# Performance work log

Measured on AMD Instinct MI355X. Metric: run time of the kernel, lower is better.

Reference implementation:

```python
import jax, jax.numpy as jnp
import numpy as np

DIM = 1024
N_HEADS = 16
HEAD_DIM = DIM // N_HEADS


def setup_inputs() -> dict:
    key = jax.random.key(0)
    k_x, k_qkv_w, k_qkv_b, k_p_w, k_p_b = jax.random.split(key, 5)
    s = 1.0 / np.sqrt(DIM)
    return {
        "x": jax.random.normal(k_x, (2, 2048, DIM), dtype=jnp.float32),
        # stored as [in, out] so forward is x @ W + b (equivalent to torch Linear)
        "qkv_w": jax.random.uniform(k_qkv_w, (DIM, 3 * DIM), minval=-s, maxval=s, dtype=jnp.float32),
        "qkv_b": jax.random.uniform(k_qkv_b, (3 * DIM,), minval=-s, maxval=s, dtype=jnp.float32),
        "proj_w": jax.random.uniform(k_p_w, (DIM, DIM), minval=-s, maxval=s, dtype=jnp.float32),
        "proj_b": jax.random.uniform(k_p_b, (DIM,), minval=-s, maxval=s, dtype=jnp.float32),
    }


def reference(x, qkv_w, qkv_b, proj_w, proj_b):
    b, s, _ = x.shape
    qkv = x @ qkv_w + qkv_b                       # [b, s, 3*dim]
    q, k, v = jnp.split(qkv, 3, axis=-1)
    def split_heads(t):
        return t.reshape(b, s, N_HEADS, HEAD_DIM).transpose(0, 2, 1, 3)  # [b, h, s, d]
    q, k, v = map(split_heads, (q, k, v))
    scale = 1.0 / np.sqrt(HEAD_DIM)
    scores = jnp.einsum("bhqd,bhkd->bhqk", q, k) * scale
    attn = jax.nn.softmax(scores, axis=-1)
    out = jnp.einsum("bhqk,bhkd->bhqd", attn, v)
    out = out.transpose(0, 2, 1, 3).reshape(b, s, DIM)
    return out @ proj_w + proj_b
```

## Files before the change

### kernel.cpp

```cpp
#include <hip/hip_runtime.h>
#include <hip/hip_bf16.h>

typedef __attribute__((ext_vector_type(8))) short bf16x8;
typedef __attribute__((ext_vector_type(4))) float f32x4;
typedef __attribute__((ext_vector_type(16))) float f32x16;
typedef __attribute__((ext_vector_type(4))) unsigned short u16x4;
typedef __attribute__((ext_vector_type(8))) unsigned short u16x8v;

#define S_LEN 2048
#define NHEAD 16
#define HDIM 64
#define DIM 1024

__device__ __forceinline__ unsigned short f2bf(float f) {
    union { float f; unsigned u; } x; x.f = f;
    unsigned r = x.u + 0x7FFFu + ((x.u >> 16) & 1u);
    return (unsigned short)(r >> 16);
}
__device__ __forceinline__ unsigned short f2bf_fast(float f) {
    union { float f; unsigned u; } x; x.f = f;
    return (unsigned short)((x.u + 0x8000u) >> 16);
}

__device__ __forceinline__ f32x4 mfma16(bf16x8 a, bf16x8 b, f32x4 c) {
    return __builtin_amdgcn_mfma_f32_16x16x32_bf16(a, b, c, 0, 0, 0);
}
__device__ __forceinline__ f32x16 mfma32(bf16x8 a, bf16x8 b, f32x16 c) {
    return __builtin_amdgcn_mfma_f32_32x32x16_bf16(a, b, c, 0, 0, 0);
}

__device__ __forceinline__ float fexp2(float x) {
#if __has_builtin(__builtin_amdgcn_exp2f)
    return __builtin_amdgcn_exp2f(x);
#else
    return exp2f(x);
#endif
}

__device__ __forceinline__ void gl_lds16(const void* g, void* l) {
    __builtin_amdgcn_global_load_lds(
        (const __attribute__((address_space(1))) unsigned int*)g,
        (__attribute__((address_space(3))) unsigned int*)l, 16, 0, 0);
}

__global__ __launch_bounds__(256) void xconv_kernel(const float* __restrict__ X,
                                                    unsigned short* __restrict__ Xb) {
    size_t i = ((size_t)blockIdx.x * 256 + threadIdx.x) * 8;
    float4 a = *reinterpret_cast<const float4*>(&X[i]);
    float4 b = *reinterpret_cast<const float4*>(&X[i + 4]);
    u16x8v o;
    o[0] = f2bf(a.x); o[1] = f2bf(a.y); o[2] = f2bf(a.z); o[3] = f2bf(a.w);
    o[4] = f2bf(b.x); o[5] = f2bf(b.y); o[6] = f2bf(b.z); o[7] = f2bf(b.w);
    *reinterpret_cast<u16x8v*>(&Xb[i]) = o;
}

__global__ __launch_bounds__(256) void wtrans_kernel(const float* __restrict__ W,
                                                     unsigned short* __restrict__ Wt,
                                                     int K, int N) {
    __shared__ float lds[64][65];
    int k0 = blockIdx.x * 64, n0 = blockIdx.y * 64;
    int tid = threadIdx.x;
    for (int idx = tid; idx < 1024; idx += 256) {
        int row = idx >> 4, c = (idx & 15) << 2;
        float4 v = *reinterpret_cast<const float4*>(&W[(size_t)(k0 + row) * N + n0 + c]);
        lds[row][c] = v.x; lds[row][c + 1] = v.y; lds[row][c + 2] = v.z; lds[row][c + 3] = v.w;
    }
    __syncthreads();
    for (int idx = tid; idx < 1024; idx += 256) {
        int row = idx >> 4, c = (idx & 15) << 2;
        u16x4 o;
        o[0] = f2bf(lds[c][row]);     o[1] = f2bf(lds[c + 1][row]);
        o[2] = f2bf(lds[c + 2][row]); o[3] = f2bf(lds[c + 3][row]);
        *reinterpret_cast<u16x4*>(&Wt[(size_t)(n0 + row) * K + k0 + c]) = o;
    }
}

template <int MODE>
__global__ __launch_bounds__(256) void gemm_kernel(
    const unsigned short* __restrict__ Ab, const unsigned short* __restrict__ Bt,
    const float* __restrict__ bias,
    unsigned short* __restrict__ Qb, unsigned short* __restrict__ Kb,
    unsigned short* __restrict__ Vt, float* __restrict__ outf) {
    __shared__ unsigned short Alds[128 * 64];
    __shared__ unsigned short Blds[128 * 64];
    const int tid = threadIdx.x;
    const int m0 = blockIdx.x * 128, n0 = blockIdx.y * 128;
    const int wid = tid >> 6, lane = tid & 63;
    const int wm = wid >> 1, wn = wid & 1;
    const int lr = lane & 15, lg = lane >> 4;

    const char* Abase = (const char*)(Ab + (size_t)m0 * 1024);
    const char* Bbase = (const char*)(Bt + (size_t)n0 * 1024);

    int srcOff[4], dstOff[4];
#pragma unroll
    for (int i = 0; i < 4; ++i) {
        int off = i * 4096 + wid * 1024 + lane * 16;
        int row = off >> 7, col = off & 127;
        srcOff[i] = row * 2048 + (col ^ ((row & 7) << 4));
        dstOff[i] = off;
    }
    const int swz = (lr & 7) << 4;

    f32x4 acc[4][4] = {};

    for (int kt = 0; kt < 16; ++kt) {
        __syncthreads();
#pragma unroll
        for (int i = 0; i < 4; ++i) {
            gl_lds16(Abase + srcOff[i] + kt * 128, (char*)Alds + dstOff[i]);
            gl_lds16(Bbase + srcOff[i] + kt * 128, (char*)Blds + dstOff[i]);
        }
        __syncthreads();

#pragma unroll
        for (int ks = 0; ks < 2; ++ks) {
            bf16x8 af[4], bfr[4];
#pragma unroll
            for (int i = 0; i < 4; ++i)
                af[i] = *reinterpret_cast<const bf16x8*>(
                    (const char*)Alds + (wm * 64 + i * 16 + lr) * 128 + ((ks * 64 + lg * 16) ^ swz));
#pragma unroll
            for (int j = 0; j < 4; ++j)
                bfr[j] = *reinterpret_cast<const bf16x8*>(
                    (const char*)Blds + (wn * 64 + j * 16 + lr) * 128 + ((ks * 64 + lg * 16) ^ swz));
            __builtin_amdgcn_s_setprio(1);
#pragma unroll
            for (int i = 0; i < 4; ++i)
#pragma unroll
                for (int j = 0; j < 4; ++j)
                    acc[i][j] = mfma16(af[i], bfr[j], acc[i][j]);
            __builtin_amdgcn_s_setprio(0);
        }
    }

    if constexpr (MODE == 0) {
        const int sec = n0 >> 10;
#pragma unroll
        for (int j = 0; j < 4; ++j) {
            int gn = n0 + wn * 64 + j * 16 + lr;
            float bv = bias[gn];
            int nn = gn & 1023, h = nn >> 6, d = nn & 63;
#pragma unroll
            for (int i = 0; i < 4; ++i) {
#pragma unroll
                for (int r = 0; r < 4; ++r) {
                    int m = m0 + wm * 64 + i * 16 + lg * 4 + r;
                    int b_ = m >> 11, s_ = m & 2047;
                    size_t bh = (size_t)(b_ * NHEAD + h);
                    float v = acc[i][j][r] + bv;
                    if (sec == 0)
                        Qb[(bh * S_LEN + s_) * HDIM + d] = f2bf(v * 0.18033688f);
                    else if (sec == 1)
                        Kb[(bh * S_LEN + s_) * HDIM + d] = f2bf(v);
                    else
                        Vt[(bh * HDIM + d) * S_LEN + s_] = f2bf(v);
                }
            }
        }
    } else {
#pragma unroll
        for (int j = 0; j < 4; ++j) {
            int gn = n0 + wn * 64 + j * 16 + lr;
            float bv = bias[gn];
#pragma unroll
            for (int i = 0; i < 4; ++i) {
#pragma unroll
                for (int r = 0; r < 4; ++r) {
                    int m = m0 + wm * 64 + i * 16 + lg * 4 + r;
                    outf[(size_t)m * DIM + gn] = acc[i][j][r] + bv;
                }
            }
        }
    }
}

#define NT (S_LEN / 64)
__global__ __launch_bounds__(256) void attn_kernel(const unsigned short* __restrict__ Qb,
                                                   const unsigned short* __restrict__ Kb,
                                                   const unsigned short* __restrict__ Vt,
                                                   unsigned short* __restrict__ Ob) {
    __shared__ unsigned short Klds[2][64 * 64];
    __shared__ unsigned short Vlds[2][64 * 64];
    const int bh = blockIdx.y;
    const int wid = threadIdx.x >> 6;
    const int lane = threadIdx.x & 63;
    const int l31 = lane & 31, hi = lane >> 5;
    const int q0 = blockIdx.x * 128 + wid * 32;

    const unsigned short* qrow = &Qb[((size_t)bh * S_LEN + q0 + l31) * HDIM];
    bf16x8 qf[4];
#pragma unroll
    for (int kst = 0; kst < 4; ++kst)
        qf[kst] = *reinterpret_cast<const bf16x8*>(&qrow[kst * 16 + hi * 8]);

    const char* kT = (const char*)&Kb[(size_t)bh * S_LEN * HDIM];
    const char* vT = (const char*)&Vt[(size_t)bh * HDIM * S_LEN];

    const int Lb0 = (wid * 2 + 0) * 1024 + lane * 16;
    const int Lb1 = (wid * 2 + 1) * 1024 + lane * 16;
    const int row0 = Lb0 >> 7, row1 = Lb1 >> 7;
    const int sw0 = (Lb0 & 127) ^ ((row0 & 7) << 4);
    const int sw1 = (Lb1 & 127) ^ ((row1 & 7) << 4);
    const int dst0 = wid * 2048, dst1 = wid * 2048 + 1024;

    const int swz = (l31 & 7) << 4;

    float ls = 0.f;
    f32x16 acc[2] = {};

    {
        char* kl = (char*)Klds[0]; char* vl = (char*)Vlds[0];
        gl_lds16(kT + row0 * 128 + sw0, kl + dst0);
        gl_lds16(kT + row1 * 128 + sw1, kl + dst1);
        gl_lds16(vT + row0 * 4096 + sw0, vl + dst0);
        gl_lds16(vT + row1 * 4096 + sw1, vl + dst1);
    }

    int cur = 0;
    for (int jt = 0; jt < NT; ++jt) {
        __syncthreads();
        if (jt + 1 < NT) {
            char* kl = (char*)Klds[cur ^ 1]; char* vl = (char*)Vlds[cur ^ 1];
            size_t kof = (size_t)(jt + 1) * 8192, vof = (size_t)(jt + 1) * 128;
            gl_lds16(kT + kof + row0 * 128 + sw0, kl + dst0);
            gl_lds16(kT + kof + row1 * 128 + sw1, kl + dst1);
            gl_lds16(vT + vof + row0 * 4096 + sw0, vl + dst0);
            gl_lds16(vT + vof + row1 * 4096 + sw1, vl + dst1);
        }
        const char* kl = (const char*)Klds[cur];
        const char* vl = (const char*)Vlds[cur];

        f32x16 p[2] = {};
        __builtin_amdgcn_s_setprio(1);
#pragma unroll
        for (int ct = 0; ct < 2; ++ct) {
            const char* krow = kl + (ct * 32 + l31) * 128;
#pragma unroll
            for (int kst = 0; kst < 4; ++kst) {
                bf16x8 kb = *reinterpret_cast<const bf16x8*>(krow + ((kst * 32 + hi * 16) ^ swz));
                p[ct] = mfma32(kb, qf[kst], p[ct]);
            }
        }
        __builtin_amdgcn_s_setprio(0);

#pragma unroll
        for (int ct = 0; ct < 2; ++ct)
#pragma unroll
            for (int r = 0; r < 16; ++r) {
                float e = fexp2(p[ct][r]);
                p[ct][r] = e;
                ls += e;
            }

        bf16x8 pa[4];
#pragma unroll
        for (int kst = 0; kst < 4; ++kst) {
            const int ctq = kst >> 1, rb = 8 * (kst & 1);
            unsigned aw[2], bw[2];
#pragma unroll
            for (int u = 0; u < 2; ++u) {
                unsigned a, b;
                asm("v_cvt_pk_bf16_f32 %0, %1, %2"
                    : "=v"(a) : "v"(p[ctq][rb + 2 * u]), "v"(p[ctq][rb + 2 * u + 1]));
                asm("v_cvt_pk_bf16_f32 %0, %1, %2"
                    : "=v"(b) : "v"(p[ctq][rb + 4 + 2 * u]), "v"(p[ctq][rb + 4 + 2 * u + 1]));
                asm volatile("v_permlane32_swap_b32 %0, %1" : "+v"(a), "+v"(b));
                aw[u] = a; bw[u] = b;
            }
            union { unsigned w[4]; bf16x8 v; } pu;
            pu.w[0] = aw[0]; pu.w[1] = aw[1]; pu.w[2] = bw[0]; pu.w[3] = bw[1];
            pa[kst] = pu.v;
        }

        __builtin_amdgcn_s_setprio(1);
#pragma unroll
        for (int dt = 0; dt < 2; ++dt) {
            const char* vrow = vl + (dt * 32 + l31) * 128;
#pragma unroll
            for (int kst = 0; kst < 4; ++kst) {
                bf16x8 vb = *reinterpret_cast<const bf16x8*>(vrow + ((kst * 32 + hi * 16) ^ swz));
                acc[dt] = mfma32(pa[kst], vb, acc[dt]);
            }
        }
        __builtin_amdgcn_s_setprio(0);

        __syncthreads();
        cur ^= 1;
    }

    ls += __shfl_xor(ls, 32, 64);

    float inv[16];
#pragma unroll
    for (int r = 0; r < 16; ++r) {
        int rq = (r & 3) + 8 * (r >> 2) + 4 * hi;
        inv[r] = 1.f / __shfl(ls, rq, 64);
    }

    const int b_ = bh >> 4, h = bh & 15;
#pragma unroll
    for (int dt = 0; dt < 2; ++dt)
#pragma unroll
        for (int r = 0; r < 16; ++r) {
            int rq = (r & 3) + 8 * (r >> 2) + 4 * hi;
            float o = acc[dt][r] * inv[r];
            int q = q0 + rq;
            Ob[((size_t)(b_ * S_LEN + q)) * DIM + h * HDIM + dt * 32 + l31] = f2bf_fast(o);
        }
}

extern "C" void kernel_launch(void* const* d_in, const int* in_sizes, int n_in,
                              void* d_out, int out_size, void* d_ws, size_t ws_size,
                              hipStream_t stream) {
    const float* x      = (const float*)d_in[0];
    const float* qkv_w  = (const float*)d_in[1];
    const float* qkv_b  = (const float*)d_in[2];
    const float* proj_w = (const float*)d_in[3];
    const float* proj_b = (const float*)d_in[4];
    float* out = (float*)d_out;

    unsigned short* Wqkvt = (unsigned short*)d_ws;
    unsigned short* Wpt   = Wqkvt + 3072 * 1024;
    unsigned short* Qb    = Wpt + 1024 * 1024;
    unsigned short* Kb    = Qb + 32 * 2048 * 64;
    unsigned short* Vt    = Kb + 32 * 2048 * 64;
    unsigned short* Ob    = Vt + 32 * 2048 * 64;
    unsigned short* Xb    = Ob + 4096 * 1024;

    xconv_kernel<<<2048, 256, 0, stream>>>(x, Xb);
    wtrans_kernel<<<dim3(16, 48), 256, 0, stream>>>(qkv_w, Wqkvt, 1024, 3072);
    wtrans_kernel<<<dim3(16, 16), 256, 0, stream>>>(proj_w, Wpt, 1024, 1024);

    gemm_kernel<0><<<dim3(32, 24), 256, 0, stream>>>(Xb, Wqkvt, qkv_b, Qb, Kb, Vt, nullptr);
    attn_kernel<<<dim3(16, 32), 256, 0, stream>>>(Qb, Kb, Vt, Ob);
    gemm_kernel<1><<<dim3(32, 8), 256, 0, stream>>>(Ob, Wpt, proj_b, nullptr, nullptr, nullptr, out);
}
```

Before: 120.7 us.

## Process two query tiles per wave in attention and remap blocks across XCDs

Each wave now handles 64 query rows (two 32-row groups) against every K/V tile loaded into LDS, halving K/V staging traffic per query and doubling MFMA work per LDS read. Blocks are remapped so heads spread across XCDs for L2 locality, and the LDS layout switches to a fragment-ordered arrangement that avoids XOR swizzle arithmetic. The grid drops to 256 blocks, which reduces parallelism and occupancy and raises register pressure from the doubled accumulators.

Result: slower. 138.5 us (+14.7%).

```diff
diff --git a/kernel.cpp b/kernel.cpp
--- a/kernel.cpp
+++ b/kernel.cpp
@@ -182,121 +182,148 @@
                                                    unsigned short* __restrict__ Ob) {
     __shared__ unsigned short Klds[2][64 * 64];
     __shared__ unsigned short Vlds[2][64 * 64];
-    const int bh = blockIdx.y;
+    const int L = blockIdx.x;
+    const int xcd = L & 7, slot = L >> 3;
+    const int bh = xcd + 8 * (slot & 3);
+    const int qblk = slot >> 2;
     const int wid = threadIdx.x >> 6;
     const int lane = threadIdx.x & 63;
     const int l31 = lane & 31, hi = lane >> 5;
-    const int q0 = blockIdx.x * 128 + wid * 32;
-
-    const unsigned short* qrow = &Qb[((size_t)bh * S_LEN + q0 + l31) * HDIM];
-    bf16x8 qf[4];
-#pragma unroll
-    for (int kst = 0; kst < 4; ++kst)
-        qf[kst] = *reinterpret_cast<const bf16x8*>(&qrow[kst * 16 + hi * 8]);
+    const int q0 = qblk * 256 + wid * 64;
+
+    const unsigned short* qrA = &Qb[((size_t)bh * S_LEN + q0 + l31) * HDIM];
+    bf16x8 qfA[4], qfB[4];
+#pragma unroll
+    for (int kst = 0; kst < 4; ++kst) {
+        qfA[kst] = *reinterpret_cast<const bf16x8*>(&qrA[kst * 16 + hi * 8]);
+        qfB[kst] = *reinterpret_cast<const bf16x8*>(&qrA[32 * HDIM + kst * 16 + hi * 8]);
+    }
 
     const char* kT = (const char*)&Kb[(size_t)bh * S_LEN * HDIM];
     const char* vT = (const char*)&Vt[(size_t)bh * HDIM * S_LEN];
 
-    const int Lb0 = (wid * 2 + 0) * 1024 + lane * 16;
-    const int Lb1 = (wid * 2 + 1) * 1024 + lane * 16;
-    const int row0 = Lb0 >> 7, row1 = Lb1 >> 7;
-    const int sw0 = (Lb0 & 127) ^ ((row0 & 7) << 4);
-    const int sw1 = (Lb1 & 127) ^ ((row1 & 7) << 4);
-    const int dst0 = wid * 2048, dst1 = wid * 2048 + 1024;
-
-    const int swz = (l31 & 7) << 4;
-
-    float ls = 0.f;
-    f32x16 acc[2] = {};
-
-    {
-        char* kl = (char*)Klds[0]; char* vl = (char*)Vlds[0];
-        gl_lds16(kT + row0 * 128 + sw0, kl + dst0);
-        gl_lds16(kT + row1 * 128 + sw1, kl + dst1);
-        gl_lds16(vT + row0 * 4096 + sw0, vl + dst0);
-        gl_lds16(vT + row1 * 4096 + sw1, vl + dst1);
-    }
+    const int c0 = 2 * wid, c1 = 2 * wid + 1;
+    const int ks0 = ((c0 >> 2) * 32 + l31) * 128 + (c0 & 3) * 32 + hi * 16;
+    const int ks1 = ((c1 >> 2) * 32 + l31) * 128 + (c1 & 3) * 32 + hi * 16;
+    const int vs0 = ((c0 >> 2) * 32 + l31) * 4096 + (c0 & 3) * 32 + hi * 16;
+    const int vs1 = ((c1 >> 2) * 32 + l31) * 4096 + (c1 & 3) * 32 + hi * 16;
+    const int du0 = c0 * 1024, du1 = c1 * 1024;
+
+    float lsA = 0.f, lsB = 0.f;
+    f32x16 accA[2] = {}, accB[2] = {};
+
+    gl_lds16(kT + ks0, (char*)Klds[0] + du0);
+    gl_lds16(kT + ks1, (char*)Klds[0] + du1);
+    gl_lds16(vT + vs0, (char*)Vlds[0] + du0);
+    gl_lds16(vT + vs1, (char*)Vlds[0] + du1);
+    __syncthreads();
 
     int cur = 0;
     for (int jt = 0; jt < NT; ++jt) {
-        __syncthreads();
         if (jt + 1 < NT) {
             char* kl = (char*)Klds[cur ^ 1]; char* vl = (char*)Vlds[cur ^ 1];
             size_t kof = (size_t)(jt + 1) * 8192, vof = (size_t)(jt + 1) * 128;
-            gl_lds16(kT + kof + row0 * 128 + sw0, kl + dst0);
-            gl_lds16(kT + kof + row1 * 128 + sw1, kl + dst1);
-            gl_lds16(vT + vof + row0 * 4096 + sw0, vl + dst0);
-            gl_lds16(vT + vof + row1 * 4096 + sw1, vl + dst1);
-        }
-        const char* kl = (const char*)Klds[cur];
-        const char* vl = (const char*)Vlds[cur];
-
-        f32x16 p[2] = {};
-        __builtin_amdgcn_s_setprio(1);
-#pragma unroll
-        for (int ct = 0; ct < 2; ++ct) {
-            const char* krow = kl + (ct * 32 + l31) * 128;
+            gl_lds16(kT + kof + ks0, kl + du0);
+            gl_lds16(kT + kof + ks1, kl + du1);
+            gl_lds16(vT + vof + vs0, vl + du0);
+            gl_lds16(vT + vof + vs1, vl + du1);
+        }
+        const char* kl = (const char*)Klds[cur] + lane * 16;
+        const char* vl = (const char*)Vlds[cur] + lane * 16;
+
+        f32x16 pA0 = {}, pA1 = {}, pB0 = {}, pB1 = {};
+#pragma unroll
+        for (int kst = 0; kst < 4; ++kst) {
+            bf16x8 kb0 = *reinterpret_cast<const bf16x8*>(kl + kst * 1024);
+            bf16x8 kb1 = *reinterpret_cast<const bf16x8*>(kl + (4 + kst) * 1024);
+            pA0 = mfma32(kb0, qfA[kst], pA0);
+            pB0 = mfma32(kb0, qfB[kst], pB0);
+            pA1 = mfma32(kb1, qfA[kst], pA1);
+            pB1 = mfma32(kb1, qfB[kst], pB1);
+        }
+
+        bf16x8 paA[4];
+        {
+#pragma unroll
+            for (int r = 0; r < 16; ++r) {
+                float e0 = fexp2(pA0[r]); pA0[r] = e0; lsA += e0;
+                float e1 = fexp2(pA1[r]); pA1[r] = e1; lsA += e1;
+            }
 #pragma unroll
             for (int kst = 0; kst < 4; ++kst) {
-                bf16x8 kb = *reinterpret_cast<const bf16x8*>(krow + ((kst * 32 + hi * 16) ^ swz));
-                p[ct] = mfma32(kb, qf[kst], p[ct]);
-            }
-        }
-        __builtin_amdgcn_s_setprio(0);
-
-#pragma unroll
-        for (int ct = 0; ct < 2; ++ct)
+                const int rb = 8 * (kst & 1);
+                unsigned aw[2], bw[2];
+#pragma unroll
+                for (int u = 0; u < 2; ++u) {
+                    unsigned a, b;
+                    if (kst < 2) {
+                        asm("v_cvt_pk_bf16_f32 %0, %1, %2" : "=v"(a) : "v"(pA0[rb + 2 * u]), "v"(pA0[rb + 2 * u + 1]));
+                        asm("v_cvt_pk_bf16_f32 %0, %1, %2" : "=v"(b) : "v"(pA0[rb + 4 + 2 * u]), "v"(pA0[rb + 4 + 2 * u + 1]));
+                    } else {
+                        asm("v_cvt_pk_bf16_f32 %0, %1, %2" : "=v"(a) : "v"(pA1[rb + 2 * u]), "v"(pA1[rb + 2 * u + 1]));
+                        asm("v_cvt_pk_bf16_f32 %0, %1, %2" : "=v"(b) : "v"(pA1[rb + 4 + 2 * u]), "v"(pA1[rb + 4 + 2 * u + 1]));
+                    }
+                    asm volatile("v_permlane32_swap_b32 %0, %1" : "+v"(a), "+v"(b));
+                    aw[u] = a; bw[u] = b;
+                }
+                union { unsigned w[4]; bf16x8 v; } pu;
+                pu.w[0] = aw[0]; pu.w[1] = aw[1]; pu.w[2] = bw[0]; pu.w[3] = bw[1];
+                paA[kst] = pu.v;
+            }
+        }
+
+#pragma unroll
+        for (int kst = 0; kst < 4; ++kst) {
+            bf16x8 vb0 = *reinterpret_cast<const bf16x8*>(vl + kst * 1024);
+            bf16x8 vb1 = *reinterpret_cast<const bf16x8*>(vl + (4 + kst) * 1024);
+            accA[0] = mfma32(paA[kst], vb0, accA[0]);
+            accA[1] = mfma32(paA[kst], vb1, accA[1]);
+        }
+
+        bf16x8 paB[4];
+        {
 #pragma unroll
             for (int r = 0; r < 16; ++r) {
-                float e = fexp2(p[ct][r]);
-                p[ct][r] = e;
-                ls += e;
-            }
-
-        bf16x8 pa[4];
+                float e0 = fexp2(pB0[r]); pB0[r] = e0; lsB += e0;
+                float e1 = fexp2(pB1[r]); pB1[r] = e1; lsB += e1;
+            }
+#pragma unroll
+            for (int kst = 0; kst < 4; ++kst) {
+                const int rb = 8 * (kst & 1);
+                unsigned aw[2], bw[2];
+#pragma unroll
+                for (int u = 0; u < 2; ++u) {
+                    unsigned a, b;
+                    if (kst < 2) {
+                        asm("v_cvt_pk_bf16_f32 %0, %1, %2" : "=v"(a) : "v"(pB0[rb + 2 * u]), "v"(pB0[rb + 2 * u + 1]));
+                        asm("v_cvt_pk_bf16_f32 %0, %1, %2" : "=v"(b) : "v"(pB0[rb + 4 + 2 * u]), "v"(pB0[rb + 4 + 2 * u + 1]));
+                    } else {
+                        asm("v_cvt_pk_bf16_f32 %0, %1, %2" : "=v"(a) : "v"(pB1[rb + 2 * u]), "v"(pB1[rb + 2 * u + 1]));
+                        asm("v_cvt_pk_bf16_f32 %0, %1, %2" : "=v"(b) : "v"(pB1[rb + 4 + 2 * u]), "v"(pB1[rb + 4 + 2 * u + 1]));
+                    }
+                    asm volatile("v_permlane32_swap_b32 %0, %1" : "+v"(a), "+v"(b));
+                    aw[u] = a; bw[u] = b;
+                }
+                union { unsigned w[4]; bf16x8 v; } pu;
+                pu.w[0] = aw[0]; pu.w[1] = aw[1]; pu.w[2] = bw[0]; pu.w[3] = bw[1];
+                paB[kst] = pu.v;
+            }
+        }
+
 #pragma unroll
         for (int kst = 0; kst < 4; ++kst) {
-            const int ctq = kst >> 1, rb = 8 * (kst & 1);
-            unsigned aw[2], bw[2];
-#pragma unroll
-            for (int u = 0; u < 2; ++u) {
-                unsigned a, b;
-                asm("v_cvt_pk_bf16_f32 %0, %1, %2"
-                    : "=v"(a) : "v"(p[ctq][rb + 2 * u]), "v"(p[ctq][rb + 2 * u + 1]));
-                asm("v_cvt_pk_bf16_f32 %0, %1, %2"
-                    : "=v"(b) : "v"(p[ctq][rb + 4 + 2 * u]), "v"(p[ctq][rb + 4 + 2 * u + 1]));
-                asm volatile("v_permlane32_swap_b32 %0, %1" : "+v"(a), "+v"(b));
-                aw[u] = a; bw[u] = b;
-            }
-            union { unsigned w[4]; bf16x8 v; } pu;
-            pu.w[0] = aw[0]; pu.w[1] = aw[1]; pu.w[2] = bw[0]; pu.w[3] = bw[1];
-            pa[kst] = pu.v;
-        }
-
-        __builtin_amdgcn_s_setprio(1);
-#pragma unroll
-        for (int dt = 0; dt < 2; ++dt) {
-            const char* vrow = vl + (dt * 32 + l31) * 128;
-#pragma unroll
-            for (int kst = 0; kst < 4; ++kst) {
-                bf16x8 vb = *reinterpret_cast<const bf16x8*>(vrow + ((kst * 32 + hi * 16) ^ swz));
-                acc[dt] = mfma32(pa[kst], vb, acc[dt]);
-            }
-        }
-        __builtin_amdgcn_s_setprio(0);
+            bf16x8 vb0 = *reinterpret_cast<const bf16x8*>(vl + kst * 1024);
+            bf16x8 vb1 = *reinterpret_cast<const bf16x8*>(vl + (4 + kst) * 1024);
+            accB[0] = mfma32(paB[kst], vb0, accB[0]);
+            accB[1] = mfma32(paB[kst], vb1, accB[1]);
+        }
 
         __syncthreads();
         cur ^= 1;
     }
 
-    ls += __shfl_xor(ls, 32, 64);
-
-    float inv[16];
-#pragma unroll
-    for (int r = 0; r < 16; ++r) {
-        int rq = (r & 3) + 8 * (r >> 2) + 4 * hi;
-        inv[r] = 1.f / __shfl(ls, rq, 64);
-    }
+    lsA += __shfl_xor(lsA, 32, 64);
+    lsB += __shfl_xor(lsB, 32, 64);
 
     const int b_ = bh >> 4, h = bh & 15;
 #pragma unroll
@@ -304,9 +331,11 @@
 #pragma unroll
         for (int r = 0; r < 16; ++r) {
             int rq = (r & 3) + 8 * (r >> 2) + 4 * hi;
-            float o = acc[dt][r] * inv[r];
-            int q = q0 + rq;
-            Ob[((size_t)(b_ * S_LEN + q)) * DIM + h * HDIM + dt * 32 + l31] = f2bf_fast(o);
+            float oA = accA[dt][r] / __shfl(lsA, rq, 64);
+            float oB = accB[dt][r] / __shfl(lsB, rq, 64);
+            int qA = q0 + rq, qB = q0 + 32 + rq;
+            Ob[((size_t)(b_ * S_LEN + qA)) * DIM + h * HDIM + dt * 32 + l31] = f2bf_fast(oA);
+            Ob[((size_t)(b_ * S_LEN + qB)) * DIM + h * HDIM + dt * 32 + l31] = f2bf_fast(oB);
         }
 }
 
@@ -333,6 +362,6 @@
     wtrans_kernel<<<dim3(16, 16), 256, 0, stream>>>(proj_w, Wpt, 1024, 1024);
 
     gemm_kernel<0><<<dim3(32, 24), 256, 0, stream>>>(Xb, Wqkvt, qkv_b, Qb, Kb, Vt, nullptr);
-    attn_kernel<<<dim3(16, 32), 256, 0, stream>>>(Qb, Kb, Vt, Ob);
+    attn_kernel<<<256, 256, 0, stream>>>(Qb, Kb, Vt, Ob);
     gemm_kernel<1><<<dim3(32, 8), 256, 0, stream>>>(Ob, Wpt, proj_b, nullptr, nullptr, nullptr, out);
 }
```

## Remap attention blocks to XCDs and store K/V in LDS in fragment order

Applied to the files above, without the earlier changes.

The attention grid becomes a flat 512-block launch, and each block's (head, query-block) pair is derived so that all query blocks of one head land on the same XCD, improving L2 reuse of that head's K/V. K and V tiles are now written into LDS already laid out per MFMA fragment, so each lane reads a contiguous 16-byte slice at lane*16 with no XOR swizzle. The loop-top barrier moves so that one sync after the prologue and one at the end of each iteration cover the double buffer. The global loads become 16-byte strided row segments, which may coalesce less well than the previous 128-byte row reads.

New measurement: 121.9 us. About the same (+1.0%).

```diff
diff --git a/kernel.cpp b/kernel.cpp
--- a/kernel.cpp
+++ b/kernel.cpp
@@ -182,11 +182,14 @@
                                                    unsigned short* __restrict__ Ob) {
     __shared__ unsigned short Klds[2][64 * 64];
     __shared__ unsigned short Vlds[2][64 * 64];
-    const int bh = blockIdx.y;
+    const int L = blockIdx.x;
+    const int xcd = L & 7, slot = L >> 3;
+    const int bh = xcd + 8 * (slot & 3);
+    const int qblk = slot >> 2;
     const int wid = threadIdx.x >> 6;
     const int lane = threadIdx.x & 63;
     const int l31 = lane & 31, hi = lane >> 5;
-    const int q0 = blockIdx.x * 128 + wid * 32;
+    const int q0 = qblk * 128 + wid * 32;
 
     const unsigned short* qrow = &Qb[((size_t)bh * S_LEN + q0 + l31) * HDIM];
     bf16x8 qf[4];
@@ -197,51 +200,44 @@
     const char* kT = (const char*)&Kb[(size_t)bh * S_LEN * HDIM];
     const char* vT = (const char*)&Vt[(size_t)bh * HDIM * S_LEN];
 
-    const int Lb0 = (wid * 2 + 0) * 1024 + lane * 16;
-    const int Lb1 = (wid * 2 + 1) * 1024 + lane * 16;
-    const int row0 = Lb0 >> 7, row1 = Lb1 >> 7;
-    const int sw0 = (Lb0 & 127) ^ ((row0 & 7) << 4);
-    const int sw1 = (Lb1 & 127) ^ ((row1 & 7) << 4);
-    const int dst0 = wid * 2048, dst1 = wid * 2048 + 1024;
-
-    const int swz = (l31 & 7) << 4;
+    const int c0 = 2 * wid, c1 = 2 * wid + 1;
+    const int ks0 = ((c0 >> 2) * 32 + l31) * 128 + (c0 & 3) * 32 + hi * 16;
+    const int ks1 = ((c1 >> 2) * 32 + l31) * 128 + (c1 & 3) * 32 + hi * 16;
+    const int vs0 = ((c0 >> 2) * 32 + l31) * 4096 + (c0 & 3) * 32 + hi * 16;
+    const int vs1 = ((c1 >> 2) * 32 + l31) * 4096 + (c1 & 3) * 32 + hi * 16;
+    const int du0 = c0 * 1024, du1 = c1 * 1024;
 
     float ls = 0.f;
     f32x16 acc[2] = {};
 
-    {
-        char* kl = (char*)Klds[0]; char* vl = (char*)Vlds[0];
-        gl_lds16(kT + row0 * 128 + sw0, kl + dst0);
-        gl_lds16(kT + row1 * 128 + sw1, kl + dst1);
-        gl_lds16(vT + row0 * 4096 + sw0, vl + dst0);
-        gl_lds16(vT + row1 * 4096 + sw1, vl + dst1);
-    }
+    gl_lds16(kT + ks0, (char*)Klds[0] + du0);
+    gl_lds16(kT + ks1, (char*)Klds[0] + du1);
+    gl_lds16(vT + vs0, (char*)Vlds[0] + du0);
+    gl_lds16(vT + vs1, (char*)Vlds[0] + du1);
+    __syncthreads();
 
     int cur = 0;
     for (int jt = 0; jt < NT; ++jt) {
-        __syncthreads();
         if (jt + 1 < NT) {
             char* kl = (char*)Klds[cur ^ 1]; char* vl = (char*)Vlds[cur ^ 1];
             size_t kof = (size_t)(jt + 1) * 8192, vof = (size_t)(jt + 1) * 128;
-            gl_lds16(kT + kof + row0 * 128 + sw0, kl + dst0);
-            gl_lds16(kT + kof + row1 * 128 + sw1, kl + dst1);
-            gl_lds16(vT + vof + row0 * 4096 + sw0, vl + dst0);
-            gl_lds16(vT + vof + row1 * 4096 + sw1, vl + dst1);
-        }
-        const char* kl = (const char*)Klds[cur];
-        const char* vl = (const char*)Vlds[cur];
+            gl_lds16(kT + kof + ks0, kl + du0);
+            gl_lds16(kT + kof + ks1, kl + du1);
+            gl_lds16(vT + vof + vs0, vl + du0);
+            gl_lds16(vT + vof + vs1, vl + du1);
+        }
+        const char* kl = (const char*)Klds[cur] + lane * 16;
+        const char* vl = (const char*)Vlds[cur] + lane * 16;
 
         f32x16 p[2] = {};
         __builtin_amdgcn_s_setprio(1);
 #pragma unroll
-        for (int ct = 0; ct < 2; ++ct) {
-            const char* krow = kl + (ct * 32 + l31) * 128;
+        for (int ct = 0; ct < 2; ++ct)
 #pragma unroll
             for (int kst = 0; kst < 4; ++kst) {
-                bf16x8 kb = *reinterpret_cast<const bf16x8*>(krow + ((kst * 32 + hi * 16) ^ swz));
+                bf16x8 kb = *reinterpret_cast<const bf16x8*>(kl + (ct * 4 + kst) * 1024);
                 p[ct] = mfma32(kb, qf[kst], p[ct]);
             }
-        }
         __builtin_amdgcn_s_setprio(0);
 
 #pragma unroll
@@ -275,14 +271,12 @@
 
         __builtin_amdgcn_s_setprio(1);
 #pragma unroll
-        for (int dt = 0; dt < 2; ++dt) {
-            const char* vrow = vl + (dt * 32 + l31) * 128;
+        for (int dt = 0; dt < 2; ++dt)
 #pragma unroll
             for (int kst = 0; kst < 4; ++kst) {
-                bf16x8 vb = *reinterpret_cast<const bf16x8*>(vrow + ((kst * 32 + hi * 16) ^ swz));
+                bf16x8 vb = *reinterpret_cast<const bf16x8*>(vl + (dt * 4 + kst) * 1024);
                 acc[dt] = mfma32(pa[kst], vb, acc[dt]);
             }
-        }
         __builtin_amdgcn_s_setprio(0);
 
         __syncthreads();
@@ -333,6 +327,6 @@
     wtrans_kernel<<<dim3(16, 16), 256, 0, stream>>>(proj_w, Wpt, 1024, 1024);
 
     gemm_kernel<0><<<dim3(32, 24), 256, 0, stream>>>(Xb, Wqkvt, qkv_b, Qb, Kb, Vt, nullptr);
-    attn_kernel<<<dim3(16, 32), 256, 0, stream>>>(Qb, Kb, Vt, Ob);
+    attn_kernel<<<512, 256, 0, stream>>>(Qb, Kb, Vt, Ob);
     gemm_kernel<1><<<dim3(32, 8), 256, 0, stream>>>(Ob, Wpt, proj_b, nullptr, nullptr, nullptr, out);
 }
```
